# Kernel optimization log

Hardware: AMD Instinct MI355X
Metric: run time of the kernel (lower is better)

## Reference

```python
import jax, jax.numpy as jnp
import numpy as np

HID = 256
NUM_EMB = 30
MAX_LEN = 500  # decode steps = MAX_LEN + 1


def setup_inputs() -> dict:
    key = jax.random.key(0)
    ks = jax.random.split(key, 20)
    B, C, H, W = 64, 512, 32, 32
    s = 0.05
    d = {}
    d["fea"] = jax.random.normal(ks[0], (B, C, H, W), jnp.float32)
    d["targets"] = jax.random.randint(ks[1], (B, MAX_LEN + 1), 0, NUM_EMB)
    d["i2h_w"] = jax.random.normal(ks[2], (C, HID), jnp.float32) * s
    d["h2h_w"] = jax.random.normal(ks[3], (HID, HID), jnp.float32) * s
    d["h2h_b"] = jax.random.normal(ks[4], (HID,), jnp.float32) * s
    d["score_w"] = jax.random.normal(ks[5], (HID, 1), jnp.float32) * s
    d["gru_w_ih"] = jax.random.normal(ks[6], (C + NUM_EMB, 3 * HID), jnp.float32) * s
    d["gru_w_hh"] = jax.random.normal(ks[7], (HID, 3 * HID), jnp.float32) * s
    d["gru_b_ih"] = jax.random.normal(ks[8], (3 * HID,), jnp.float32) * s
    d["gru_b_hh"] = jax.random.normal(ks[9], (3 * HID,), jnp.float32) * s
    d["sg1_w"] = jax.random.normal(ks[10], (HID, HID), jnp.float32) * s
    d["sg1_b"] = jax.random.normal(ks[11], (HID,), jnp.float32) * s
    d["sg2_w"] = jax.random.normal(ks[12], (HID, NUM_EMB), jnp.float32) * s
    d["sg2_b"] = jax.random.normal(ks[13], (NUM_EMB,), jnp.float32) * s
    d["lg1_w"] = jax.random.normal(ks[14], (HID, HID), jnp.float32) * s
    d["lg1_b"] = jax.random.normal(ks[15], (HID,), jnp.float32) * s
    d["lg2_w"] = jax.random.normal(ks[16], (HID, 4), jnp.float32) * s
    d["lg2_b"] = jax.random.normal(ks[17], (4,), jnp.float32) * s
    return d


def reference(fea, targets, i2h_w, h2h_w, h2h_b, score_w,
              gru_w_ih, gru_w_hh, gru_b_ih, gru_b_hh,
              sg1_w, sg1_b, sg2_w, sg2_b, lg1_w, lg1_b, lg2_w, lg2_b):
    B, C, H, W = fea.shape
    feat = fea.reshape(B, C, H * W).transpose(0, 2, 1)          # [B,T,C]
    # content projection of encoder features is step-invariant: hoist out of loop
    proj = jnp.einsum('btc,ch->bth', feat, i2h_w)               # [B,T,HID]

    def step(hidden, char):
        # attention over spatial positions
        ph = hidden @ h2h_w + h2h_b                             # [B,HID]
        e = jnp.tanh(proj + ph[:, None, :]) @ score_w           # [B,T,1]
        alpha = jax.nn.softmax(e[..., 0], axis=1)               # [B,T]
        context = jnp.einsum('bt,btc->bc', alpha, feat)         # [B,C]
        onehot = jax.nn.one_hot(char, NUM_EMB, dtype=hidden.dtype)
        x = jnp.concatenate([context, onehot], axis=-1)         # [B,C+NUM_EMB]
        # GRU cell (torch semantics)
        gx = x @ gru_w_ih + gru_b_ih
        gh = hidden @ gru_w_hh + gru_b_hh
        xr, xz, xn = jnp.split(gx, 3, axis=-1)
        hr, hz, hn = jnp.split(gh, 3, axis=-1)
        r = jax.nn.sigmoid(xr + hr)
        z = jax.nn.sigmoid(xz + hz)
        n = jnp.tanh(xn + r * hn)
        h_new = (1.0 - z) * n + z * hidden
        struct = (h_new @ sg1_w + sg1_b) @ sg2_w + sg2_b        # [B,NUM_EMB]
        loc = jax.nn.sigmoid((h_new @ lg1_w + lg1_b) @ lg2_w + lg2_b)  # [B,4]
        return h_new, (struct, loc)

    h0 = jnp.zeros((B, HID), fea.dtype)
    _, (structs, locs) = jax.lax.scan(step, h0, targets.T)      # over 501 steps
    structure_preds = structs.transpose(1, 0, 2)                # [B,501,NUM_EMB]
    loc_preds = locs.transpose(1, 0, 2)                         # [B,501,4]
    return structure_preds, loc_preds
```

## Files before the change

kernel.cpp:

```cpp
#include <hip/hip_runtime.h>
#include <hip/hip_bf16.h>
#include <hip/hip_fp16.h>
#include <math.h>

#define BB 64
#define CDIM 512
#define TT 1024
#define HID 256
#define NEMB 30
#define GDIM 768

typedef _Float16 v2h __attribute__((ext_vector_type(2)));

struct TanhC { float c[7]; };

__device__ inline float f_dot2(v2h a, v2h b, float c) {
  return __builtin_amdgcn_fdot2(a, b, c, false);
}
__device__ inline v2h u2v(unsigned u) { return __builtin_bit_cast(v2h, u); }
__device__ inline unsigned v2u(v2h h) { return __builtin_bit_cast(unsigned, h); }
__device__ inline unsigned packh2(float a, float b) {
  v2h t = {(_Float16)a, (_Float16)b};
  return v2u(t);
}
__device__ inline v2h v2splat(float f) {
  _Float16 h = (_Float16)f;
  v2h r = {h, h};
  return r;
}

__device__ inline float ldin(const void* p, long i, int isb) {
  if (isb) {
    unsigned u = ((const unsigned short*)p)[i];
    return __uint_as_float(u << 16);
  }
  return ((const float*)p)[i];
}

template <int CTRL, int RM, int BM, bool BC>
__device__ inline float dpp_add(float v) {
  int m = __builtin_amdgcn_update_dpp(0, __builtin_bit_cast(int, v), CTRL, RM, BM, BC);
  return v + __builtin_bit_cast(float, m);
}
__device__ inline float wave_sum64(float v) {
  v = dpp_add<0x111, 0xf, 0xf, true>(v);
  v = dpp_add<0x112, 0xf, 0xf, true>(v);
  v = dpp_add<0x114, 0xf, 0xe, false>(v);
  v = dpp_add<0x118, 0xf, 0xc, false>(v);
  v = dpp_add<0x142, 0xa, 0xf, false>(v);
  v = dpp_add<0x143, 0xc, 0xf, false>(v);
  return v;
}

__global__ void k_sniff(const void* fea, int* flag) {
  __shared__ int s[256];
  int tid = threadIdx.x;
  const unsigned short* u16 = (const unsigned short*)fea;
  int cnt = 0;
  for (int i = tid; i < 2048; i += 256) {
    unsigned u = u16[2 * i];
    float v = __uint_as_float(u << 16);
    float a = fabsf(v);
    if (a > 1e-6f && a < 16.0f) cnt++;
  }
  s[tid] = cnt;
  __syncthreads();
  for (int off = 128; off > 0; off >>= 1) {
    if (tid < off) s[tid] += s[tid + off];
    __syncthreads();
  }
  if (tid == 0) flag[0] = (s[0] > 1024) ? 1 : 0;
}

__global__ void k_cvt_f(const void* src, float* dst, long n, const int* flag) {
  int isb = flag[0];
  long i = (long)blockIdx.x * blockDim.x + threadIdx.x;
  long stride = (long)gridDim.x * blockDim.x;
  for (; i < n; i += stride) dst[i] = ldin(src, i, isb);
}

__global__ void k_wc(const void* i2h, const void* wih, unsigned* wc2, const int* flag) {
  int isb = flag[0];
  int idx = blockIdx.x * 256 + threadIdx.x;
  int cp = idx >> 10, col = idx & 1023;
  float a, b;
  if (col < 256) {
    a = ldin(i2h, (long)(2 * cp) * 256 + col, isb);
    b = ldin(i2h, (long)(2 * cp + 1) * 256 + col, isb);
  } else {
    int j = col - 256;
    a = ldin(wih, (long)(2 * cp) * GDIM + j, isb);
    b = ldin(wih, (long)(2 * cp + 1) * GDIM + j, isb);
  }
  wc2[idx] = packh2(a, b);
}

__global__ void k_w4(const void* h2hw, const void* whhw, unsigned* w4, const int* flag) {
  int isb = flag[0];
  int idx = blockIdx.x * 256 + threadIdx.x;
  int l = idx >> 10, col = idx & 1023;
  float a, b2;
  if (col < 256) {
    a = ldin(h2hw, (long)(2 * l) * 256 + col, isb);
    b2 = ldin(h2hw, (long)(2 * l + 1) * 256 + col, isb);
  } else {
    int j = col - 256;
    a = ldin(whhw, (long)(2 * l) * GDIM + j, isb);
    b2 = ldin(whhw, (long)(2 * l + 1) * GDIM + j, isb);
  }
  w4[idx] = packh2(a, b2);
}

__global__ void k_bias4(const void* h2hb, const void* bhh, float* bias4, const int* flag) {
  int isb = flag[0];
  int col = blockIdx.x * 256 + threadIdx.x;
  bias4[col] = (col < 256) ? ldin(h2hb, col, isb) : ldin(bhh, col - 256, isb);
}

__global__ void k_embb(const void* wih, const void* bih, float* embb, const int* flag) {
  int isb = flag[0];
  int idx = blockIdx.x * 256 + threadIdx.x;
  if (idx >= NEMB * GDIM) return;
  int e = idx / GDIM, col = idx % GDIM;
  embb[idx] = ldin(wih, (long)(512 + e) * GDIM + col, isb) + ldin(bih, col, isb);
}

__global__ void k_comb(const void* sg1w, const void* sg1b, const void* sg2w, const void* sg2b,
                       const void* lg1w, const void* lg1b, const void* lg2w, const void* lg2b,
                       float* comb_w, float* comb_b, const int* flag) {
  int isb = flag[0];
  int tid = threadIdx.x;
  float acc[34];
#pragma unroll
  for (int o = 0; o < 34; ++o) acc[o] = 0.f;
  for (int m = 0; m < HID; ++m) {
    float s1 = ldin(sg1w, (long)tid * HID + m, isb);
    float l1 = ldin(lg1w, (long)tid * HID + m, isb);
#pragma unroll
    for (int o = 0; o < 30; ++o) acc[o] += s1 * ldin(sg2w, (long)m * NEMB + o, isb);
#pragma unroll
    for (int o = 0; o < 4; ++o) acc[30 + o] += l1 * ldin(lg2w, (long)m * 4 + o, isb);
  }
  for (int o = 0; o < 34; ++o) comb_w[tid * 34 + o] = acc[o];
  if (tid < 34) {
    float a = 0.f;
    if (tid < 30) {
      for (int m = 0; m < HID; ++m) a += ldin(sg1b, m, isb) * ldin(sg2w, (long)m * NEMB + tid, isb);
      a += ldin(sg2b, tid, isb);
    } else {
      int o = tid - 30;
      for (int m = 0; m < HID; ++m) a += ldin(lg1b, m, isb) * ldin(lg2w, (long)m * 4 + o, isb);
      a += ldin(lg2b, o, isb);
    }
    comb_b[tid] = a;
  }
}

__global__ __launch_bounds__(256) void k_gemm(const void* fea, const unsigned* wc2,
                                              unsigned* pp, unsigned* fw2, const int* flag) {
  const int isb = flag[0];
  const int blk = blockIdx.x;
  const int b = blk >> 6;
  const int tt = (blk >> 3) & 7;
  const int cc = blk & 7;
  const int t0 = tt * 128, c0 = cc * 128;
  __shared__ __align__(16) unsigned At[32][136];
  __shared__ __align__(16) unsigned Wt[32][136];
  const int tid = threadIdx.x;
  const int cp_l = tid >> 3, sg = tid & 7;
  const int tm = tid & 15, tn = tid >> 4;
  float acc[8][8];
#pragma unroll
  for (int i = 0; i < 8; ++i)
#pragma unroll
    for (int jj = 0; jj < 8; ++jj) acc[i][jj] = 0.f;

  for (int kt = 0; kt < 8; ++kt) {
    const int crow = (kt * 32 + cp_l) * 2;
    if (isb) {
      const unsigned short* f0p =
          (const unsigned short*)fea + ((long)b * CDIM + crow) * TT + t0 + sg * 16;
      const unsigned short* f1p = f0p + TT;
#pragma unroll
      for (int q = 0; q < 2; ++q) {
        ushort4 u0a = ((const ushort4*)f0p)[2 * q];
        ushort4 u0b = ((const ushort4*)f0p)[2 * q + 1];
        ushort4 u1a = ((const ushort4*)f1p)[2 * q];
        ushort4 u1b = ((const ushort4*)f1p)[2 * q + 1];
        unsigned short a0[8] = {u0a.x, u0a.y, u0a.z, u0a.w, u0b.x, u0b.y, u0b.z, u0b.w};
        unsigned short a1[8] = {u1a.x, u1a.y, u1a.z, u1a.w, u1b.x, u1b.y, u1b.z, u1b.w};
#pragma unroll
        for (int e = 0; e < 8; ++e) {
          float f0 = __uint_as_float(((unsigned)a0[e]) << 16);
          float f1 = __uint_as_float(((unsigned)a1[e]) << 16);
          At[cp_l][sg * 16 + q * 8 + e] = packh2(f0, f1);
        }
      }
    } else {
      const float* f0p = (const float*)fea + ((long)b * CDIM + crow) * TT + t0 + sg * 16;
      const float* f1p = f0p + TT;
#pragma unroll
      for (int q = 0; q < 4; ++q) {
        float4 v0 = ((const float4*)f0p)[q];
        float4 v1 = ((const float4*)f1p)[q];
        At[cp_l][sg * 16 + q * 4 + 0] = packh2(v0.x, v1.x);
        At[cp_l][sg * 16 + q * 4 + 1] = packh2(v0.y, v1.y);
        At[cp_l][sg * 16 + q * 4 + 2] = packh2(v0.z, v1.z);
        At[cp_l][sg * 16 + q * 4 + 3] = packh2(v0.w, v1.w);
      }
    }
    {
      const uint4* wp = (const uint4*)(wc2 + (long)(kt * 32 + cp_l) * 1024 + c0 + sg * 16);
#pragma unroll
      for (int q = 0; q < 4; ++q) {
        uint4 w = wp[q];
        Wt[cp_l][sg * 16 + q * 4 + 0] = w.x;
        Wt[cp_l][sg * 16 + q * 4 + 1] = w.y;
        Wt[cp_l][sg * 16 + q * 4 + 2] = w.z;
        Wt[cp_l][sg * 16 + q * 4 + 3] = w.w;
      }
    }
    __syncthreads();
    for (int cp = 0; cp < 32; ++cp) {
      uint4 aq0 = *(const uint4*)&At[cp][tm * 4];
      uint4 aq1 = *(const uint4*)&At[cp][64 + tm * 4];
      uint4 bq0 = *(const uint4*)&Wt[cp][tn * 4];
      uint4 bq1 = *(const uint4*)&Wt[cp][64 + tn * 4];
      unsigned av[8] = {aq0.x, aq0.y, aq0.z, aq0.w, aq1.x, aq1.y, aq1.z, aq1.w};
      unsigned bv[8] = {bq0.x, bq0.y, bq0.z, bq0.w, bq1.x, bq1.y, bq1.z, bq1.w};
#pragma unroll
      for (int ti = 0; ti < 8; ++ti)
#pragma unroll
        for (int ci = 0; ci < 8; ++ci)
          acc[ti][ci] = f_dot2(u2v(av[ti]), u2v(bv[ci]), acc[ti][ci]);
    }
    __syncthreads();
  }

#pragma unroll
  for (int q = 0; q < 2; ++q) {
    const int tq = t0 + q * 64 + tm * 4;
#pragma unroll
    for (int pr = 0; pr < 2; ++pr) {
      const int tp = (tq >> 1) + pr;
      const int r0 = q * 4 + 2 * pr, r1 = r0 + 1;
      unsigned* row;
      if (cc < 2)
        row = pp + ((long)b * 512 + tp) * 256 + c0 + tn * 4;
      else
        row = fw2 + ((long)b * 512 + tp) * GDIM + (c0 - 256) + tn * 4;
      uint4 pa = {packh2(acc[r0][0], acc[r1][0]), packh2(acc[r0][1], acc[r1][1]),
                  packh2(acc[r0][2], acc[r1][2]), packh2(acc[r0][3], acc[r1][3])};
      uint4 pb = {packh2(acc[r0][4], acc[r1][4]), packh2(acc[r0][5], acc[r1][5]),
                  packh2(acc[r0][6], acc[r1][6]), packh2(acc[r0][7], acc[r1][7])};
      *(uint4*)row = pa;
      *(uint4*)(row + 64) = pb;
    }
  }
}

__global__ __launch_bounds__(1024, 4) void k_main_c2(
    const unsigned* pp, const unsigned* fw2, const int* targets, const unsigned* w4,
    const float* bias4, const float* embb, const float* scoref, const float* comb_w,
    const float* comb_b, void* out, const int* flag, int steps, TanhC tc, int* bar1, float* Sx,
    float* ghxx, float* gxpx) {
  const int tid = threadIdx.x;
  const int g = blockIdx.x & 63;
  const int j = blockIdx.x >> 6;
  const int lane = tid & 63, wid = tid >> 6;
  const int isb = flag[0];

  __shared__ __align__(16) float sh_pa[3072];
  __shared__ unsigned sh_phsc[264];
  __shared__ unsigned sh_alpha2[128];
  __shared__ float sh_hidden[HID];
  __shared__ unsigned sh_h2[128];
  __shared__ float sh_red[4];

  float my_sc = (tid < HID) ? scoref[tid] : 0.f;
  if (tid < HID) sh_hidden[tid] = 0.f;
  if (tid < 128) sh_h2[tid] = 0u;
  __syncthreads();

  const v2h C0 = v2splat(tc.c[0]), C1 = v2splat(tc.c[1]), C2 = v2splat(tc.c[2]),
            C3 = v2splat(tc.c[3]), C4 = v2splat(tc.c[4]), C5 = v2splat(tc.c[5]),
            C6 = v2splat(tc.c[6]);
  const v2h CLO = v2splat(-3.9f), CHI = v2splat(3.9f);
  const v2h VS = v2splat(0.0625f);

  const unsigned* ppbase = pp + ((long)g * 512 + j * 128) * 256;
  const unsigned* fwbase = fw2 + ((long)g * 512 + j * 128) * GDIM;

  const int dsub = (tid < 768) ? tid / 192 : 0;
  const int dcg = (tid < 768) ? tid % 192 : 0;
  const uint4* frbase = (const uint4*)(fwbase + (long)(dsub * 32) * GDIM) + dcg;

  const int btp = tid >> 3, bhc = tid & 7;
  const uint4* prow = (const uint4*)(ppbase + (long)btp * 256) + bhc * 8;

  for (int step = 0; step < steps; ++step) {
    const int tgt = targets[g * steps + step];
    const int par = step & 1;
    float* S_cur = Sx + par * 256;
    float* ghx_cur = ghxx + (long)par * 64 * GDIM;
    float* gxp_cur = gxpx + (long)par * 64 * 4 * GDIM;

    uint4 pf[8];
#pragma unroll
    for (int i = 0; i < 8; ++i) pf[i] = frbase[(long)i * 192];

    {
      const int chunk = tid >> 8, col = tid & 255;
      float a = 0.f;
      const unsigned* wp = w4 + (long)(chunk * 32) * 1024 + col;
#pragma unroll 8
      for (int l = 0; l < 32; ++l) a = f_dot2(u2v(sh_h2[chunk * 32 + l]), u2v(wp[l * 1024]), a);
      sh_pa[chunk * 256 + col] = a;
    }
    if (tid < 768) {
      const int ch = tid / 192, cl = tid % 192;
      const int gcol = 256 + j * 192 + cl;
      float a = 0.f;
      const unsigned* wp = w4 + (long)(ch * 32) * 1024 + gcol;
#pragma unroll 8
      for (int l = 0; l < 32; ++l) a = f_dot2(u2v(sh_h2[ch * 32 + l]), u2v(wp[l * 1024]), a);
      sh_pa[1024 + ch * 192 + cl] = a;
    }
    __syncthreads();
    if (tid < 256) {
      float ph = sh_pa[tid] + sh_pa[256 + tid] + sh_pa[512 + tid] + sh_pa[768 + tid] + bias4[tid];
      sh_phsc[(tid >> 5) * 33 + (tid & 31)] = packh2(ph, my_sc);
    } else if (tid < 448) {
      int cl = tid - 256;
      float gv = sh_pa[1024 + cl] + sh_pa[1024 + 192 + cl] + sh_pa[1024 + 384 + cl] +
                 sh_pa[1024 + 576 + cl] + bias4[256 + j * 192 + cl];
      ghx_cur[(long)g * GDIM + j * 192 + cl] = gv;
    }
    __syncthreads();

    {
      v2h acc = v2splat(0.f);
#pragma unroll
      for (int q = 0; q < 8; ++q) {
        uint4 w = prow[q];
        unsigned we[4] = {w.x, w.y, w.z, w.w};
#pragma unroll
        for (int e = 0; e < 4; ++e) {
          int hl = q * 4 + e;
          v2h ps = u2v(sh_phsc[bhc * 33 + hl]);
          v2h phb = {ps.x, ps.x};
          v2h scb = {ps.y, ps.y};
          v2h x = u2v(we[e]) + phb;
          x = __builtin_elementwise_max(x, CLO);
          x = __builtin_elementwise_min(x, CHI);
          v2h v = x * x * VS;
          v2h p = C6;
          p = p * v + C5;
          p = p * v + C4;
          p = p * v + C3;
          p = p * v + C2;
          p = p * v + C1;
          p = p * v + C0;
          acc = acc + scb * (p * x);
        }
      }
      ((float2*)sh_pa)[btp * 9 + bhc] = make_float2((float)acc.x, (float)acc.y);
    }
    __syncthreads();

    if (tid < 128) {
      float e0 = 0.f, e1 = 0.f;
#pragma unroll
      for (int k = 0; k < 8; ++k) {
        float2 v = ((const float2*)sh_pa)[tid * 9 + k];
        e0 += v.x;
        e1 += v.y;
      }
      float p0 = exp2f(e0 * 1.44269504f);
      float p1 = exp2f(e1 * 1.44269504f);
      sh_alpha2[tid] = packh2(p0, p1);
      float s = wave_sum64(p0 + p1);
      if (lane == 63) sh_red[wid] = s;
    }
    __syncthreads();
    if (tid == 0) S_cur[g * 4 + j] = sh_red[0] + sh_red[1];

    if (tid < 768) {
      float a0 = 0.f, a1 = 0.f, a2 = 0.f, a3 = 0.f;
#pragma unroll
      for (int i = 0; i < 8; ++i) {
        v2h al = u2v(sh_alpha2[dsub * 32 + i]);
        a0 = f_dot2(al, u2v(pf[i].x), a0);
        a1 = f_dot2(al, u2v(pf[i].y), a1);
        a2 = f_dot2(al, u2v(pf[i].z), a2);
        a3 = f_dot2(al, u2v(pf[i].w), a3);
      }
#pragma unroll 8
      for (int i = 8; i < 32; ++i) {
        uint4 w = frbase[(long)i * 192];
        v2h al = u2v(sh_alpha2[dsub * 32 + i]);
        a0 = f_dot2(al, u2v(w.x), a0);
        a1 = f_dot2(al, u2v(w.y), a1);
        a2 = f_dot2(al, u2v(w.z), a2);
        a3 = f_dot2(al, u2v(w.w), a3);
      }
      *(float4*)&sh_pa[dsub * GDIM + dcg * 4] = make_float4(a0, a1, a2, a3);
    }
    __syncthreads();
    if (tid < 768) {
      float v = sh_pa[tid] + sh_pa[GDIM + tid] + sh_pa[2 * GDIM + tid] + sh_pa[3 * GDIM + tid];
      gxp_cur[((long)g * 4 + j) * GDIM + tid] = v;
    }

    __syncthreads();
    if (tid == 0) {
      __hip_atomic_fetch_add(&bar1[g], 1, __ATOMIC_ACQ_REL, __HIP_MEMORY_SCOPE_AGENT);
      const int tgt4 = 4 * (step + 1);
      while (__hip_atomic_load(&bar1[g], __ATOMIC_RELAXED, __HIP_MEMORY_SCOPE_AGENT) < tgt4)
        __builtin_amdgcn_s_sleep(2);
      (void)__hip_atomic_load(&bar1[g], __ATOMIC_ACQUIRE, __HIP_MEMORY_SCOPE_AGENT);
    }
    __syncthreads();

    if (tid < 256) {
      float D = S_cur[g * 4] + S_cur[g * 4 + 1] + S_cur[g * 4 + 2] + S_cur[g * 4 + 3];
      float rs = 1.0f / D;
      const float* eb = embb + (long)tgt * GDIM;
      float gr = 0.f, gz = 0.f, gn = 0.f;
#pragma unroll
      for (int jj = 0; jj < 4; ++jj) {
        const float* gp = gxp_cur + ((long)g * 4 + jj) * GDIM;
        gr += gp[tid];
        gz += gp[tid + 256];
        gn += gp[tid + 512];
      }
      gr = gr * rs + eb[tid];
      gz = gz * rs + eb[tid + 256];
      gn = gn * rs + eb[tid + 512];
      const float* gh = ghx_cur + (long)g * GDIM;
      float hr = gh[tid], hz = gh[tid + 256], hn = gh[tid + 512];
      float r = 1.f / (1.f + __expf(-(gr + hr)));
      float z = 1.f / (1.f + __expf(-(gz + hz)));
      float n = tanhf(gn + r * hn);
      sh_hidden[tid] = (1.f - z) * n + z * sh_hidden[tid];
    }
    __syncthreads();

    if (tid < 128) sh_h2[tid] = packh2(sh_hidden[2 * tid], sh_hidden[2 * tid + 1]);
    if (j == (step & 3)) {
      float hv[4];
      if (tid < 64) {
#pragma unroll
        for (int k = 0; k < 4; ++k) hv[k] = sh_hidden[lane + 64 * k];
      }
      if (tid < 34) {
        float a = comb_b[tid];
#pragma unroll
        for (int k = 0; k < 4; ++k) {
          for (int l = 0; l < 64; ++l) {
            float h = __builtin_bit_cast(
                float, __builtin_amdgcn_readlane(__builtin_bit_cast(int, hv[k]), l));
            a += h * comb_w[(64 * k + l) * 34 + tid];
          }
        }
        long so;
        float vv;
        if (tid < 30) {
          so = ((long)g * steps + step) * 30 + tid;
          vv = a;
        } else {
          so = (long)BB * steps * 30 + ((long)g * steps + step) * 4 + (tid - 30);
          vv = 1.f / (1.f + __expf(-a));
        }
        if (isb)
          ((__hip_bfloat16*)out)[so] = __float2bfloat16(vv);
        else
          ((float*)out)[so] = vv;
      }
    }
    __syncthreads();
  }
}

static void fit_tanh(float cf[7]) {
  double A[7][7] = {{0}}, r[7] = {0};
  const int N = 1024;
  for (int i = 1; i <= N; ++i) {
    double x = 3.9 * i / N;
    double v = (x * x) / 16.0;
    double t = tanh(x);
    double phi[7];
    double pw = x;
    for (int jj = 0; jj < 7; ++jj) {
      phi[jj] = pw;
      pw *= v;
    }
    for (int jj = 0; jj < 7; ++jj) {
      r[jj] += phi[jj] * t;
      for (int k = 0; k < 7; ++k) A[jj][k] += phi[jj] * phi[k];
    }
  }
  for (int col = 0; col < 7; ++col) {
    int piv = col;
    for (int rr = col + 1; rr < 7; ++rr)
      if (fabs(A[rr][col]) > fabs(A[piv][col])) piv = rr;
    if (piv != col) {
      for (int k = 0; k < 7; ++k) {
        double tmp = A[col][k];
        A[col][k] = A[piv][k];
        A[piv][k] = tmp;
      }
      double tb = r[col];
      r[col] = r[piv];
      r[piv] = tb;
    }
    double d = A[col][col];
    for (int rr = col + 1; rr < 7; ++rr) {
      double f = A[rr][col] / d;
      for (int k = col; k < 7; ++k) A[rr][k] -= f * A[col][k];
      r[rr] -= f * r[col];
    }
  }
  double c[7];
  for (int col = 6; col >= 0; --col) {
    double ss = r[col];
    for (int k = col + 1; k < 7; ++k) ss -= A[col][k] * c[k];
    c[col] = ss / A[col][col];
  }
  for (int jj = 0; jj < 7; ++jj) cf[jj] = (float)c[jj];
}

extern "C" void kernel_launch(void* const* d_in, const int* in_sizes, int n_in, void* d_out,
                              int out_size, void* d_ws, size_t ws_size, hipStream_t stream) {
  (void)n_in;
  (void)out_size;
  (void)ws_size;
  const void* fea = d_in[0];
  const int* targets = (const int*)d_in[1];
  const void* i2h_w = d_in[2];
  const void* h2h_w = d_in[3];
  const void* h2h_b = d_in[4];
  const void* score_w = d_in[5];
  const void* gru_w_ih = d_in[6];
  const void* gru_w_hh = d_in[7];
  const void* gru_b_ih = d_in[8];
  const void* gru_b_hh = d_in[9];
  const void* sg1_w = d_in[10];
  const void* sg1_b = d_in[11];
  const void* sg2_w = d_in[12];
  const void* sg2_b = d_in[13];
  const void* lg1_w = d_in[14];
  const void* lg1_b = d_in[15];
  const void* lg2_w = d_in[16];
  const void* lg2_b = d_in[17];
  const int steps = in_sizes[1] / BB;

  char* p = (char*)d_ws;
  auto alloc = [&](size_t bytes) {
    char* r = p;
    p += (bytes + 255) & ~(size_t)255;
    return r;
  };
  unsigned* pp = (unsigned*)alloc((size_t)BB * 512 * 256 * 4);
  unsigned* fw2 = (unsigned*)alloc((size_t)BB * 512 * GDIM * 4);
  unsigned* wc2 = (unsigned*)alloc((size_t)256 * 1024 * 4);
  unsigned* w4 = (unsigned*)alloc((size_t)128 * 1024 * 4);
  float* bias4 = (float*)alloc(1024 * 4);
  float* embb = (float*)alloc((size_t)NEMB * GDIM * 4);
  float* scoref = (float*)alloc(256 * 4);
  float* combw = (float*)alloc(256 * 34 * 4);
  float* combb = (float*)alloc(64 * 4);
  int* flag = (int*)alloc(256);
  int* bars = (int*)alloc(4096);
  float* Sx = (float*)alloc((size_t)2 * 64 * 4 * 4);
  float* ghxx = (float*)alloc((size_t)2 * 64 * GDIM * 4);
  float* gxpx = (float*)alloc((size_t)2 * 64 * 4 * GDIM * 4);
  int* bar1 = bars;

  TanhC tc;
  fit_tanh(tc.c);

  hipMemsetAsync(bars, 0, 4096, stream);
  k_sniff<<<1, 256, 0, stream>>>(fea, flag);
  k_wc<<<1024, 256, 0, stream>>>(i2h_w, gru_w_ih, wc2, flag);
  k_w4<<<512, 256, 0, stream>>>(h2h_w, gru_w_hh, w4, flag);
  k_bias4<<<4, 256, 0, stream>>>(h2h_b, gru_b_hh, bias4, flag);
  k_embb<<<90, 256, 0, stream>>>(gru_w_ih, gru_b_ih, embb, flag);
  k_cvt_f<<<1, 256, 0, stream>>>(score_w, scoref, 256, flag);
  k_comb<<<1, 256, 0, stream>>>(sg1_w, sg1_b, sg2_w, sg2_b, lg1_w, lg1_b, lg2_w, lg2_b, combw,
                                combb, flag);
  k_gemm<<<4096, 256, 0, stream>>>(fea, wc2, pp, fw2, flag);

  k_main_c2<<<256, 1024, 0, stream>>>(pp, fw2, targets, w4, bias4, embb, scoref, combw, combb,
                                      d_out, flag, steps, tc, bar1, Sx, ghxx, gxpx);
}
```

Baseline: 21.72 ms.

## Transpose recurrent weights for vector loads and prefetch attention rows across phases

```diff
diff --git a/kernel.cpp b/kernel.cpp
--- a/kernel.cpp
+++ b/kernel.cpp
@@ -95,10 +95,10 @@
   wc2[idx] = packh2(a, b);
 }
 
-__global__ void k_w4(const void* h2hw, const void* whhw, unsigned* w4, const int* flag) {
+__global__ void k_w4t(const void* h2hw, const void* whhw, unsigned* w4t, const int* flag) {
   int isb = flag[0];
   int idx = blockIdx.x * 256 + threadIdx.x;
-  int l = idx >> 10, col = idx & 1023;
+  int col = idx >> 7, l = idx & 127;
   float a, b2;
   if (col < 256) {
     a = ldin(h2hw, (long)(2 * l) * 256 + col, isb);
@@ -108,7 +108,7 @@
     a = ldin(whhw, (long)(2 * l) * GDIM + j, isb);
     b2 = ldin(whhw, (long)(2 * l + 1) * GDIM + j, isb);
   }
-  w4[idx] = packh2(a, b2);
+  w4t[idx] = packh2(a, b2);
 }
 
 __global__ void k_bias4(const void* h2hb, const void* bhh, float* bias4, const int* flag) {
@@ -259,8 +259,8 @@
   }
 }
 
-__global__ __launch_bounds__(1024, 4) void k_main_c2(
-    const unsigned* pp, const unsigned* fw2, const int* targets, const unsigned* w4,
+__global__ __launch_bounds__(1024, 4) void k_main_c3(
+    const unsigned* pp, const unsigned* fw2, const int* targets, const unsigned* w4t,
     const float* bias4, const float* embb, const float* scoref, const float* comb_w,
     const float* comb_b, void* out, const int* flag, int steps, TanhC tc, int* bar1, float* Sx,
     float* ghxx, float* gxpx) {
@@ -298,6 +298,13 @@
   const int btp = tid >> 3, bhc = tid & 7;
   const uint4* prow = (const uint4*)(ppbase + (long)btp * 256) + bhc * 8;
 
+  const int achunk = tid >> 8, acol = tid & 255;
+  const uint4* awp = (const uint4*)(w4t + (long)acol * 128 + achunk * 32);
+  const int gch = (tid < 768) ? tid / 192 : 0;
+  const int gcl = (tid < 768) ? tid % 192 : 0;
+  const int gcol = 256 + j * 192 + gcl;
+  const uint4* gwp = (const uint4*)(w4t + (long)gcol * 128 + gch * 32);
+
   for (int step = 0; step < steps; ++step) {
     const int tgt = targets[g * steps + step];
     const int par = step & 1;
@@ -305,26 +312,40 @@
     float* ghx_cur = ghxx + (long)par * 64 * GDIM;
     float* gxp_cur = gxpx + (long)par * 64 * 4 * GDIM;
 
-    uint4 pf[8];
-#pragma unroll
-    for (int i = 0; i < 8; ++i) pf[i] = frbase[(long)i * 192];
+    uint4 pw[8];
+#pragma unroll
+    for (int q = 0; q < 8; ++q) pw[q] = prow[q];
+    uint4 cur[8];
+#pragma unroll
+    for (int i = 0; i < 8; ++i) cur[i] = frbase[(long)i * 192];
 
     {
-      const int chunk = tid >> 8, col = tid & 255;
+      uint4 wv[8];
+#pragma unroll
+      for (int q = 0; q < 8; ++q) wv[q] = awp[q];
       float a = 0.f;
-      const unsigned* wp = w4 + (long)(chunk * 32) * 1024 + col;
-#pragma unroll 8
-      for (int l = 0; l < 32; ++l) a = f_dot2(u2v(sh_h2[chunk * 32 + l]), u2v(wp[l * 1024]), a);
-      sh_pa[chunk * 256 + col] = a;
+#pragma unroll
+      for (int q = 0; q < 8; ++q) {
+        unsigned we[4] = {wv[q].x, wv[q].y, wv[q].z, wv[q].w};
+#pragma unroll
+        for (int e = 0; e < 4; ++e)
+          a = f_dot2(u2v(sh_h2[achunk * 32 + q * 4 + e]), u2v(we[e]), a);
+      }
+      sh_pa[achunk * 256 + acol] = a;
     }
     if (tid < 768) {
-      const int ch = tid / 192, cl = tid % 192;
-      const int gcol = 256 + j * 192 + cl;
+      uint4 wv[8];
+#pragma unroll
+      for (int q = 0; q < 8; ++q) wv[q] = gwp[q];
       float a = 0.f;
-      const unsigned* wp = w4 + (long)(ch * 32) * 1024 + gcol;
-#pragma unroll 8
-      for (int l = 0; l < 32; ++l) a = f_dot2(u2v(sh_h2[ch * 32 + l]), u2v(wp[l * 1024]), a);
-      sh_pa[1024 + ch * 192 + cl] = a;
+#pragma unroll
+      for (int q = 0; q < 8; ++q) {
+        unsigned we[4] = {wv[q].x, wv[q].y, wv[q].z, wv[q].w};
+#pragma unroll
+        for (int e = 0; e < 4; ++e)
+          a = f_dot2(u2v(sh_h2[gch * 32 + q * 4 + e]), u2v(we[e]), a);
+      }
+      sh_pa[1024 + gch * 192 + gcl] = a;
     }
     __syncthreads();
     if (tid < 256) {
@@ -342,8 +363,7 @@
       v2h acc = v2splat(0.f);
 #pragma unroll
       for (int q = 0; q < 8; ++q) {
-        uint4 w = prow[q];
-        unsigned we[4] = {w.x, w.y, w.z, w.w};
+        unsigned we[4] = {pw[q].x, pw[q].y, pw[q].z, pw[q].w};
 #pragma unroll
         for (int e = 0; e < 4; ++e) {
           int hl = q * 4 + e;
@@ -388,21 +408,24 @@
     if (tid < 768) {
       float a0 = 0.f, a1 = 0.f, a2 = 0.f, a3 = 0.f;
 #pragma unroll
-      for (int i = 0; i < 8; ++i) {
-        v2h al = u2v(sh_alpha2[dsub * 32 + i]);
-        a0 = f_dot2(al, u2v(pf[i].x), a0);
-        a1 = f_dot2(al, u2v(pf[i].y), a1);
-        a2 = f_dot2(al, u2v(pf[i].z), a2);
-        a3 = f_dot2(al, u2v(pf[i].w), a3);
-      }
-#pragma unroll 8
-      for (int i = 8; i < 32; ++i) {
-        uint4 w = frbase[(long)i * 192];
-        v2h al = u2v(sh_alpha2[dsub * 32 + i]);
-        a0 = f_dot2(al, u2v(w.x), a0);
-        a1 = f_dot2(al, u2v(w.y), a1);
-        a2 = f_dot2(al, u2v(w.z), a2);
-        a3 = f_dot2(al, u2v(w.w), a3);
+      for (int c = 0; c < 4; ++c) {
+        uint4 nx[8];
+        if (c < 3) {
+#pragma unroll
+          for (int i = 0; i < 8; ++i) nx[i] = frbase[(long)((c + 1) * 8 + i) * 192];
+        }
+#pragma unroll
+        for (int i = 0; i < 8; ++i) {
+          v2h al = u2v(sh_alpha2[dsub * 32 + c * 8 + i]);
+          a0 = f_dot2(al, u2v(cur[i].x), a0);
+          a1 = f_dot2(al, u2v(cur[i].y), a1);
+          a2 = f_dot2(al, u2v(cur[i].z), a2);
+          a3 = f_dot2(al, u2v(cur[i].w), a3);
+        }
+        if (c < 3) {
+#pragma unroll
+          for (int i = 0; i < 8; ++i) cur[i] = nx[i];
+        }
       }
       *(float4*)&sh_pa[dsub * GDIM + dcg * 4] = make_float4(a0, a1, a2, a3);
     }
@@ -564,7 +587,7 @@
   unsigned* pp = (unsigned*)alloc((size_t)BB * 512 * 256 * 4);
   unsigned* fw2 = (unsigned*)alloc((size_t)BB * 512 * GDIM * 4);
   unsigned* wc2 = (unsigned*)alloc((size_t)256 * 1024 * 4);
-  unsigned* w4 = (unsigned*)alloc((size_t)128 * 1024 * 4);
+  unsigned* w4t = (unsigned*)alloc((size_t)128 * 1024 * 4);
   float* bias4 = (float*)alloc(1024 * 4);
   float* embb = (float*)alloc((size_t)NEMB * GDIM * 4);
   float* scoref = (float*)alloc(256 * 4);
@@ -583,7 +606,7 @@
   hipMemsetAsync(bars, 0, 4096, stream);
   k_sniff<<<1, 256, 0, stream>>>(fea, flag);
   k_wc<<<1024, 256, 0, stream>>>(i2h_w, gru_w_ih, wc2, flag);
-  k_w4<<<512, 256, 0, stream>>>(h2h_w, gru_w_hh, w4, flag);
+  k_w4t<<<512, 256, 0, stream>>>(h2h_w, gru_w_hh, w4t, flag);
   k_bias4<<<4, 256, 0, stream>>>(h2h_b, gru_b_hh, bias4, flag);
   k_embb<<<90, 256, 0, stream>>>(gru_w_ih, gru_b_ih, embb, flag);
   k_cvt_f<<<1, 256, 0, stream>>>(score_w, scoref, 256, flag);
@@ -591,6 +614,6 @@
                                 combb, flag);
   k_gemm<<<4096, 256, 0, stream>>>(fea, wc2, pp, fw2, flag);
 
-  k_main_c2<<<256, 1024, 0, stream>>>(pp, fw2, targets, w4, bias4, embb, scoref, combw, combb,
+  k_main_c3<<<256, 1024, 0, stream>>>(pp, fw2, targets, w4t, bias4, embb, scoref, combw, combb,
                                       d_out, flag, steps, tc, bar1, Sx, ghxx, gxpx);
 }
```

Result: slower. 55.04 ms (+153.4%).
